# Performance work log

Measured on AMD Instinct MI355X. Metric: run time of the kernel, lower is better.

Reference implementation:

```python
import jax, jax.numpy as jnp
import numpy as np

IN_F = 4096
OUT_F = 4096
GROUP = 128                      # quantization group size
NG = IN_F * OUT_F // GROUP       # 131072 groups
LORA_R = 16
LORA_SCALE = 32.0 / 16.0         # lora_alpha / lora_r


def _dequant(indices, codebook, scales):
    # Unpack two INT4 nibbles per byte: low nibble first, then high (interleaved).
    low = indices & 15
    high = (indices >> 4) & 15
    idx = jnp.stack([low, high], axis=1).reshape(-1)          # [numel]
    # Codebook lookup, per-group scaling.
    vals = codebook[idx].reshape(NG, GROUP) * scales[:, None]  # [NG, GROUP]
    return vals.reshape(OUT_F, IN_F)


def setup_inputs() -> dict:
    key = jax.random.key(0)
    ks = jax.random.split(key, 7)
    return {
        "x": jax.random.normal(ks[0], (4, 2048, IN_F), dtype=jnp.float32),
        "indices": jax.random.randint(ks[1], (IN_F * OUT_F // 2,), 0, 256, dtype=jnp.int32),
        "codebook": jax.random.normal(ks[2], (16,), dtype=jnp.float32),
        "scales": jax.random.uniform(ks[3], (NG,), dtype=jnp.float32, minval=0.01, maxval=1.0),
        "lora_A": jax.random.normal(ks[4], (IN_F, LORA_R), dtype=jnp.float32) / 64.0,
        "lora_B": jax.random.normal(ks[5], (LORA_R, OUT_F), dtype=jnp.float32) / 64.0,
        "bias": jax.random.normal(ks[6], (OUT_F,), dtype=jnp.float32),
    }


def reference(x, indices, codebook, scales, lora_A, lora_B, bias):
    # lowram path: dequantize INT4 codebook weights, F.linear, fused LoRA add, bias.
    W = _dequant(indices, codebook, scales)                    # [OUT_F, IN_F]
    h = jnp.einsum('bsi,oi->bso', x, W)                        # F.linear (no bias yet)
    h = h + (x @ lora_A) @ lora_B * LORA_SCALE                 # LoRA adapter (dropout=0)
    return h + bias
```

## Files before the change

### kernel.cpp

```cpp
#include <hip/hip_runtime.h>
#include <stdint.h>

#define IN_F   4096
#define OUT_F  4096
#define M_TOT  8192
#define KDIM   4096

typedef float          f32x4  __attribute__((ext_vector_type(4)));
typedef int            i32x4  __attribute__((ext_vector_type(4)));
typedef unsigned short u16x8  __attribute__((ext_vector_type(8)));
typedef __bf16         bf16x8 __attribute__((ext_vector_type(8)));

__device__ __forceinline__ unsigned short f2bf(float f) {
  uint32_t u = __builtin_bit_cast(uint32_t, f);
  u = (u + 0x7FFFu + ((u >> 16) & 1u)) >> 16;
  return (unsigned short)u;
}

__device__ __forceinline__ void gld_lds16(const void* g, void* l) {
  __builtin_amdgcn_global_load_lds((const __attribute__((address_space(1))) void*)g,
                                   (__attribute__((address_space(3))) void*)l,
                                   16, 0, 0);
}

__global__ __launch_bounds__(256) void k_xcast(const f32x4* __restrict__ x,
                                               u16x8* __restrict__ xb) {
  int t = blockIdx.x * 256 + threadIdx.x;
  f32x4 a = x[2 * t];
  f32x4 b = x[2 * t + 1];
  u16x8 o;
  o[0] = f2bf(a[0]); o[1] = f2bf(a[1]); o[2] = f2bf(a[2]); o[3] = f2bf(a[3]);
  o[4] = f2bf(b[0]); o[5] = f2bf(b[1]); o[6] = f2bf(b[2]); o[7] = f2bf(b[3]);
  xb[t] = o;
}

__global__ __launch_bounds__(256) void k_lora(const float* __restrict__ A,
                                              const float* __restrict__ Bm,
                                              float* __restrict__ L) {
  __shared__ float sB[16][64];
  const int ib = blockIdx.x * 256;
  const int ob = blockIdx.y * 64;
  const int t  = threadIdx.x;
  for (int j = 0; j < 4; ++j) {
    int idx = t + j * 256;
    int r = idx >> 6, oc = idx & 63;
    sB[r][oc] = Bm[r * OUT_F + ob + oc];
  }
  float a[16];
  const f32x4* Ap = (const f32x4*)(A + (size_t)(ib + t) * 16);
  #pragma unroll
  for (int j = 0; j < 4; ++j) {
    f32x4 v = Ap[j];
    a[4*j+0] = v[0]; a[4*j+1] = v[1]; a[4*j+2] = v[2]; a[4*j+3] = v[3];
  }
  __syncthreads();
  float* Lp = L + (size_t)ob * IN_F + ib + t;
  #pragma unroll 4
  for (int oc = 0; oc < 64; ++oc) {
    float acc = 0.f;
    #pragma unroll
    for (int r = 0; r < 16; ++r) acc += a[r] * sB[r][oc];
    Lp[(size_t)oc * IN_F] = acc * 2.0f;
  }
}

__global__ __launch_bounds__(256) void k_dequant(const int* __restrict__ idx,
                                                 const float* __restrict__ cb,
                                                 const float* __restrict__ scales,
                                                 const float* __restrict__ L,
                                                 unsigned short* __restrict__ Wc) {
  __shared__ float scb[16];
  const int t = blockIdx.x * 256 + threadIdx.x;
  if (threadIdx.x < 16) scb[threadIdx.x] = cb[threadIdx.x];
  __syncthreads();
  i32x4 w = ((const i32x4*)idx)[t];
  float sc = scales[t >> 4];
  f32x4 l0 = ((const f32x4*)L)[2 * t];
  f32x4 l1 = ((const f32x4*)L)[2 * t + 1];
  float lv[8] = {l0[0], l0[1], l0[2], l0[3], l1[0], l1[1], l1[2], l1[3]};
  u16x8 o;
  #pragma unroll
  for (int j = 0; j < 4; ++j) {
    int word = w[j];
    float v0 = scb[word & 15] * sc + lv[2 * j];
    float v1 = scb[(word >> 4) & 15] * sc + lv[2 * j + 1];
    o[2 * j]     = f2bf(v0);
    o[2 * j + 1] = f2bf(v1);
  }
  ((u16x8*)Wc)[t] = o;
}


#define BARR()  __builtin_amdgcn_s_barrier()
#define LGKM0() asm volatile("s_waitcnt lgkmcnt(0)" ::: "memory")
#define VMC6()  asm volatile("s_waitcnt vmcnt(6)" ::: "memory")
#define VMC0()  asm volatile("s_waitcnt vmcnt(0)" ::: "memory")

#define STAGE_A(kt, ha, c) do {                                                          \
  gld_lds16(Ag + (size_t)((ha) * 128) * KDIM + (kt) * 64,                                \
            smem + (c) * 32768 + (ha) * 16384 + ldsw);                                   \
  gld_lds16(Ag + (size_t)((ha) * 128 + 64) * KDIM + (kt) * 64,                           \
            smem + (c) * 32768 + (ha) * 16384 + 8192 + ldsw);                            \
} while (0)

#define STAGE_B(kt, hb, c) do {                                                          \
  gld_lds16(Bg + (size_t)((hb) * 128) * KDIM + (kt) * 64,                                \
            smem + 65536 + (c) * 32768 + (hb) * 16384 + ldsw);                           \
  gld_lds16(Bg + (size_t)((hb) * 128 + 64) * KDIM + (kt) * 64,                           \
            smem + 65536 + (c) * 32768 + (hb) * 16384 + 8192 + ldsw);                    \
} while (0)

#define LOAD_A(qm, c) do {                                                               \
  const char* _p = smem + (c) * 32768 + rowA + (qm) * 8192;                              \
  _Pragma("unroll")                                                                      \
  for (int mi = 0; mi < 4; ++mi) {                                                       \
    af[mi][0] = *(const bf16x8*)(_p + mi * 2048 + coff0);                                \
    af[mi][1] = *(const bf16x8*)(_p + mi * 2048 + coff1);                                \
  }                                                                                      \
} while (0)

#define LOAD_B(c) do {                                                                   \
  const char* _p = smem + 65536 + (c) * 32768 + rowB;                                    \
  _Pragma("unroll")                                                                      \
  for (int ni = 0; ni < 4; ++ni) {                                                       \
    bfr[ni][0] = *(const bf16x8*)(_p + ni * 2048 + coff0);                               \
    bfr[ni][1] = *(const bf16x8*)(_p + ni * 2048 + coff1);                               \
  }                                                                                      \
} while (0)

#define MFMA_PH(qm, nb) do {                                                             \
  __builtin_amdgcn_s_setprio(1);                                                         \
  _Pragma("unroll")                                                                      \
  for (int mi = 0; mi < 4; ++mi)                                                         \
    _Pragma("unroll")                                                                    \
    for (int nj = 0; nj < 2; ++nj)                                                       \
      _Pragma("unroll")                                                                  \
      for (int kk = 0; kk < 2; ++kk)                                                     \
        acc[(qm) * 4 + mi][(nb) * 2 + nj] = __builtin_amdgcn_mfma_f32_16x16x32_bf16(     \
            af[mi][kk], bfr[(nb) * 2 + nj][kk], acc[(qm) * 4 + mi][(nb) * 2 + nj],       \
            0, 0, 0);                                                                    \
  __builtin_amdgcn_s_setprio(0);                                                         \
} while (0)

#define TILE(t_, c_, doS4, doS123, VMCODE) do {                                          \
                                                                                \
  LOAD_A(0, c_); LOAD_B(c_);                                                             \
  if (doS4) STAGE_A((t_) + 1, 1, (c_) ^ 1);                                              \
  BARR(); LGKM0(); MFMA_PH(0, 0); BARR();                                                \
                                                                                \
  if (doS123) STAGE_B((t_) + 2, 0, c_);                                                  \
  BARR(); MFMA_PH(0, 1); BARR();                                                         \
                                                                                \
  LOAD_A(1, c_);                                                                         \
  if (doS123) STAGE_B((t_) + 2, 1, c_);                                                  \
  BARR(); LGKM0(); MFMA_PH(1, 1); BARR();                                                \
                                                                                \
  if (doS123) STAGE_A((t_) + 2, 0, c_);                                                  \
  BARR(); MFMA_PH(1, 0); VMCODE; BARR();                                                 \
} while (0)

__global__ __launch_bounds__(512, 2) void k_gemm(const unsigned short* __restrict__ A,
                                                 const unsigned short* __restrict__ B,
                                                 const float* __restrict__ bias,
                                                 float* __restrict__ C) {
  __shared__ char smem[131072];
  const int tid  = threadIdx.x;
  const int lane = tid & 63;
  const int wv   = tid >> 6;
  const int wm   = wv >> 2;
  const int wn   = wv & 3;
  const int r    = lane & 15;
  const int q    = lane >> 4;
  const int xr   = r & 7;
  const int coff0 = (q ^ xr) << 4;
  const int coff1 = ((q + 4) ^ xr) << 4;
  const int rowA = (wm * 128 + r) * 128;
  const int rowB = (wn * 64 + r) * 128;
  const int srow = tid >> 3;
  const int scol = ((tid & 7) ^ ((tid >> 3) & 7)) * 8;
  const int ldsw = wv * 1024;
  const int bm = blockIdx.x;
  const int bn = blockIdx.y;

  const unsigned short* Ag = A + (size_t)(bm * 256 + srow) * KDIM + scol;
  const unsigned short* Bg = B + (size_t)(bn * 256 + srow) * KDIM + scol;

  bf16x8 af[4][2], bfr[4][2];
  f32x4 acc[8][4];
  #pragma unroll
  for (int m = 0; m < 8; ++m)
    #pragma unroll
    for (int n = 0; n < 4; ++n)
      acc[m][n] = (f32x4){0.f, 0.f, 0.f, 0.f};

  STAGE_B(0, 0, 0); STAGE_B(0, 1, 0); STAGE_A(0, 0, 0); STAGE_A(0, 1, 0);
  STAGE_B(1, 0, 1); STAGE_B(1, 1, 1); STAGE_A(1, 0, 1);
  VMC6();
  BARR();

  #pragma unroll 1
  for (int t = 0; t < 62; t += 2) {
    TILE(t,     0, 1, 1, VMC6());
    TILE(t + 1, 1, 1, 1, VMC6());
  }
  TILE(62, 0, 1, 0, VMC0());
  TILE(63, 1, 0, 0, VMC0());

  const int row0 = bm * 256 + wm * 128;
  const int col0 = bn * 256 + wn * 64;
  float bv[4];
  #pragma unroll
  for (int ni = 0; ni < 4; ++ni) bv[ni] = bias[col0 + ni * 16 + r];
  #pragma unroll
  for (int mi = 0; mi < 8; ++mi) {
    #pragma unroll
    for (int j = 0; j < 4; ++j) {
      const int row = row0 + mi * 16 + q * 4 + j;
      float* Cp = C + (size_t)row * OUT_F + col0 + r;
      #pragma unroll
      for (int ni = 0; ni < 4; ++ni)
        Cp[ni * 16] = acc[mi][ni][j] + bv[ni];
    }
  }
}

extern "C" void kernel_launch(void* const* d_in, const int* in_sizes, int n_in,
                              void* d_out, int out_size, void* d_ws, size_t ws_size,
                              hipStream_t stream) {
  const float* x    = (const float*)d_in[0];
  const int*   idx  = (const int*)d_in[1];
  const float* cb   = (const float*)d_in[2];
  const float* scl  = (const float*)d_in[3];
  const float* lA   = (const float*)d_in[4];
  const float* lB   = (const float*)d_in[5];
  const float* bias = (const float*)d_in[6];
  float* out = (float*)d_out;

  unsigned short* xb = (unsigned short*)d_ws;
  unsigned short* Wc = (unsigned short*)((char*)d_ws + (size_t)M_TOT * KDIM * 2);
  float* Lbuf = out;

  k_xcast<<<16384, 256, 0, stream>>>((const f32x4*)x, (u16x8*)xb);
  k_lora<<<dim3(16, 64), 256, 0, stream>>>(lA, lB, Lbuf);
  k_dequant<<<8192, 256, 0, stream>>>(idx, cb, scl, Lbuf, Wc);
  k_gemm<<<dim3(32, 16), 512, 0, stream>>>(xb, Wc, bias, out);
}
```

Baseline: 289.8 us.

## Store LoRA delta in bf16 and stage GEMM epilogue through LDS for vector stores

The LoRA delta buffer is now written and read as bf16 rather than fp32, which halves that intermediate's traffic in the lora and dequant kernels. The GEMM epilogue now transposes each accumulator tile through per-wave LDS scratch so every thread can write 16-byte vectors of contiguous output columns with the bias added. The bf16 delta adds one extra rounding step before the weights are rounded to bf16 anyway. The epilogue adds a block barrier and LDS round trips in exchange for wider, coalesced global stores.

```diff
diff --git a/kernel.cpp b/kernel.cpp
--- a/kernel.cpp
+++ b/kernel.cpp
@@ -15,6 +15,9 @@
   uint32_t u = __builtin_bit_cast(uint32_t, f);
   u = (u + 0x7FFFu + ((u >> 16) & 1u)) >> 16;
   return (unsigned short)u;
+}
+__device__ __forceinline__ float bf2f(unsigned short s) {
+  return __builtin_bit_cast(float, (uint32_t)s << 16);
 }
 
 __device__ __forceinline__ void gld_lds16(const void* g, void* l) {
@@ -36,7 +39,7 @@
 
 __global__ __launch_bounds__(256) void k_lora(const float* __restrict__ A,
                                               const float* __restrict__ Bm,
-                                              float* __restrict__ L) {
+                                              unsigned short* __restrict__ L) {
   __shared__ float sB[16][64];
   const int ib = blockIdx.x * 256;
   const int ob = blockIdx.y * 64;
@@ -54,20 +57,20 @@
     a[4*j+0] = v[0]; a[4*j+1] = v[1]; a[4*j+2] = v[2]; a[4*j+3] = v[3];
   }
   __syncthreads();
-  float* Lp = L + (size_t)ob * IN_F + ib + t;
+  unsigned short* Lp = L + (size_t)ob * IN_F + ib + t;
   #pragma unroll 4
   for (int oc = 0; oc < 64; ++oc) {
     float acc = 0.f;
     #pragma unroll
     for (int r = 0; r < 16; ++r) acc += a[r] * sB[r][oc];
-    Lp[(size_t)oc * IN_F] = acc * 2.0f;
+    Lp[(size_t)oc * IN_F] = f2bf(acc * 2.0f);
   }
 }
 
 __global__ __launch_bounds__(256) void k_dequant(const int* __restrict__ idx,
                                                  const float* __restrict__ cb,
                                                  const float* __restrict__ scales,
-                                                 const float* __restrict__ L,
+                                                 const unsigned short* __restrict__ L,
                                                  unsigned short* __restrict__ Wc) {
   __shared__ float scb[16];
   const int t = blockIdx.x * 256 + threadIdx.x;
@@ -75,15 +78,13 @@
   __syncthreads();
   i32x4 w = ((const i32x4*)idx)[t];
   float sc = scales[t >> 4];
-  f32x4 l0 = ((const f32x4*)L)[2 * t];
-  f32x4 l1 = ((const f32x4*)L)[2 * t + 1];
-  float lv[8] = {l0[0], l0[1], l0[2], l0[3], l1[0], l1[1], l1[2], l1[3]};
+  u16x8 lw = ((const u16x8*)L)[t];
   u16x8 o;
   #pragma unroll
   for (int j = 0; j < 4; ++j) {
     int word = w[j];
-    float v0 = scb[word & 15] * sc + lv[2 * j];
-    float v1 = scb[(word >> 4) & 15] * sc + lv[2 * j + 1];
+    float v0 = scb[word & 15] * sc + bf2f(lw[2 * j]);
+    float v1 = scb[(word >> 4) & 15] * sc + bf2f(lw[2 * j + 1]);
     o[2 * j]     = f2bf(v0);
     o[2 * j + 1] = f2bf(v1);
   }
@@ -206,20 +207,29 @@
   TILE(62, 0, 1, 0, VMC0());
   TILE(63, 1, 0, 0, VMC0());
 
-  const int row0 = bm * 256 + wm * 128;
-  const int col0 = bn * 256 + wn * 64;
-  float bv[4];
-  #pragma unroll
-  for (int ni = 0; ni < 4; ++ni) bv[ni] = bias[col0 + ni * 16 + r];
-  #pragma unroll
-  for (int mi = 0; mi < 8; ++mi) {
+  __syncthreads();
+  {
+    char* eps = smem + wv * 4096;
+    const int row0 = bm * 256 + wm * 128;
+    const int col0 = bn * 256 + wn * 64;
+    const f32x4 bias4 = *(const f32x4*)(bias + col0 + r * 4);
     #pragma unroll
-    for (int j = 0; j < 4; ++j) {
-      const int row = row0 + mi * 16 + q * 4 + j;
-      float* Cp = C + (size_t)row * OUT_F + col0 + r;
+    for (int mi = 0; mi < 8; ++mi) {
       #pragma unroll
-      for (int ni = 0; ni < 4; ++ni)
-        Cp[ni * 16] = acc[mi][ni][j] + bv[ni];
+      for (int j = 0; j < 4; ++j)
+        #pragma unroll
+        for (int ni = 0; ni < 4; ++ni)
+          *(float*)(eps + (((q * 4 + j) * 64) + ni * 16 + r) * 4) = acc[mi][ni][j];
+      LGKM0();
+      __builtin_amdgcn_sched_barrier(0);
+      #pragma unroll
+      for (int p = 0; p < 4; ++p) {
+        const int row = p * 4 + q;
+        f32x4 v = *(const f32x4*)(eps + row * 256 + r * 16);
+        v[0] += bias4[0]; v[1] += bias4[1]; v[2] += bias4[2]; v[3] += bias4[3];
+        *(f32x4*)(C + (size_t)(row0 + mi * 16 + row) * OUT_F + col0 + r * 4) = v;
+      }
+      asm volatile("" ::: "memory");
     }
   }
 }
@@ -238,7 +248,7 @@
 
   unsigned short* xb = (unsigned short*)d_ws;
   unsigned short* Wc = (unsigned short*)((char*)d_ws + (size_t)M_TOT * KDIM * 2);
-  float* Lbuf = out;
+  unsigned short* Lbuf = (unsigned short*)d_out;
 
   k_xcast<<<16384, 256, 0, stream>>>((const f32x4*)x, (u16x8*)xb);
   k_lora<<<dim3(16, 64), 256, 0, stream>>>(lA, lB, Lbuf);
```

New measurement: 282.6 us. 2.5% less time.
